# Kernel tuning notes

Hardware: AMD Instinct MI355X
Metric: run time of the kernel (lower is better)

The kernel has to match this reference:

```python
import jax, jax.numpy as jnp
import numpy as np

N_INP = 256
N_OUT = 16
H = 1024
UH = 32  # uni_hidden_unit
BATCH = 16384


def setup_inputs() -> dict:
    key = jax.random.key(0)
    ks = jax.random.split(key, 16)
    s = 0.02
    return {
        "x": jax.random.normal(ks[0], (BATCH, N_INP), dtype=jnp.float32),
        # main MLP: n_inp -> 1024 -> 1024 -> n_out
        "W0": jax.random.normal(ks[1], (N_INP, H), dtype=jnp.float32) * s,
        "b0": jnp.zeros((H,), jnp.float32),
        "W1": jax.random.normal(ks[2], (H, H), dtype=jnp.float32) * s,
        "b1": jnp.zeros((H,), jnp.float32),
        "W2": jax.random.normal(ks[3], (H, N_OUT), dtype=jnp.float32) * s,
        "b2": jnp.zeros((N_OUT,), jnp.float32),
        # stacked per-feature uni MLPs: 1 -> UH -> UH -> n_out, one per feature
        "uw1": jax.random.normal(ks[4], (N_INP, UH), dtype=jnp.float32) * s,
        "ub1": jnp.zeros((N_INP, UH), jnp.float32),
        "uw2": jax.random.normal(ks[5], (N_INP, UH, UH), dtype=jnp.float32) * s,
        "ub2": jnp.zeros((N_INP, UH), jnp.float32),
        "uw3": jax.random.normal(ks[6], (N_INP, UH, N_OUT), dtype=jnp.float32) * s,
        "ub3": jnp.zeros((N_INP, N_OUT), jnp.float32),
    }


def reference(x, W0, b0, W1, b1, W2, b2, uw1, ub1, uw2, ub2, uw3, ub3):
    # main MLP: Linear+ReLU, Linear+ReLU, Linear
    y = jax.nn.relu(x @ W0 + b0)
    y = jax.nn.relu(y @ W1 + b1)
    y = y @ W2 + b2  # [B, n_out]

    # per-feature univariate MLPs, vectorized over the feature axis i
    # input to uni MLP i is x[:, i:i+1]  -> first Linear(1, UH)
    h = jax.nn.relu(x[:, :, None] * uw1[None] + ub1[None])       # [B, I, UH]
    h = jax.nn.relu(jnp.einsum('bif,ifo->bio', h, uw2) + ub2[None])  # [B, I, UH]
    u = jnp.einsum('bif,ifo->bio', h, uw3) + ub3[None]           # [B, I, n_out]
    return y + u.sum(axis=1)
```

## Files before the change

kernel.cpp:

```cpp
#include <hip/hip_runtime.h>

typedef unsigned short u16;
typedef __attribute__((ext_vector_type(4))) float f32x4;
typedef __attribute__((ext_vector_type(4))) int i32x4;
typedef __attribute__((ext_vector_type(8))) __bf16 bf16x8;
typedef __attribute__((ext_vector_type(4))) unsigned short u16x4;

#define BATCH 16384
#define NINP 256
#define HID 1024
#define NOUT 16

__device__ __forceinline__ u16 f2bf(float f) {
  unsigned u = __builtin_bit_cast(unsigned, f);
  u += 0x7FFFu + ((u >> 16) & 1u);
  return (u16)(u >> 16);
}
__device__ __forceinline__ f32x4 mfma_bb(bf16x8 a, bf16x8 b, f32x4 c) {
  return __builtin_amdgcn_mfma_f32_16x16x32_bf16(a, b, c, 0, 0, 0);
}
__device__ __forceinline__ void gload_lds16(const void* g, void* l) {
  __builtin_amdgcn_global_load_lds(
      (const __attribute__((address_space(1))) void*)g,
      (__attribute__((address_space(3))) void*)l, 16, 0, 0);
}

static const size_t OFF_H0    = 0;
static const size_t OFF_PARTU = 0;
static const size_t OFF_XB    = 33554432;
static const size_t OFF_PARTF = 33554432;
static const size_t OFF_W0T   = 67108864;
static const size_t OFF_W1T   = 67633152;
static const size_t OFF_W2T   = 69730304;
static const size_t OFF_UWP   = 69763072;
static const size_t OFF_CB    = 70811648;

__global__ __launch_bounds__(256) void k_prep(
    const float* __restrict__ x,
    const float* __restrict__ W0, const float* __restrict__ W1,
    const float* __restrict__ W2,
    const float* __restrict__ uw1, const float* __restrict__ ub1,
    const float* __restrict__ uw2, const float* __restrict__ ub2,
    const float* __restrict__ uw3, const float* __restrict__ b2,
    const float* __restrict__ ub3,
    u16* __restrict__ xb,
    u16* __restrict__ W0T, u16* __restrict__ W1T, u16* __restrict__ W2T,
    char* __restrict__ uwp, float* __restrict__ cb)
{
  __shared__ float tile[32][33];
  const int bid = blockIdx.x;
  const int tid = threadIdx.x;

  if (bid < 1312) {
    const float* src; u16* dst; int K, N, kb, ob;
    if (bid < 256)       { src = W0; dst = W0T; K = 256;  N = 1024; int t = bid;        kb = (t & 7) * 32;  ob = (t >> 3) * 32; }
    else if (bid < 1280) { src = W1; dst = W1T; K = 1024; N = 1024; int t = bid - 256;  kb = (t & 31) * 32; ob = (t >> 5) * 32; }
    else                 { src = W2; dst = W2T; K = 1024; N = 16;   int t = bid - 1280; kb = t * 32;        ob = 0; }
    const int tx = tid & 31, ty = tid >> 5;
    for (int r = ty; r < 32; r += 8)
      if (ob + tx < N) tile[r][tx] = src[(size_t)(kb + r) * N + ob + tx];
    __syncthreads();
    for (int r = ty; r < 32; r += 8)
      if (ob + r < N) dst[(size_t)(ob + r) * K + kb + tx] = f2bf(tile[tx][r]);
  } else if (bid < 5408) {
    const int idx = ((bid - 1312) * 256 + tid) * 4;
    const float4 v = *(const float4*)&x[idx];
    u16x4 o4 = { f2bf(v.x), f2bf(v.y), f2bf(v.z), f2bf(v.w) };
    *(u16x4*)&xb[idx] = o4;
  } else if (bid < 5664) {
    const int e = ((bid - 5408) * 256 + tid) * 4;
    const float4 v = *(const float4*)&uw2[e];
    const int i = e >> 10, f = (e >> 5) & 31, o = e & 31;
    const float vv[4] = { v.x, v.y, v.z, v.w };
    u16* blob16 = (u16*)(uwp + (size_t)i * 4096);
#pragma unroll
    for (int d = 0; d < 4; ++d) {
      const int oo = o + d;
      const int lane = ((f >> 3) << 4) | (oo & 15);
      blob16[256 + (oo >> 4) * 512 + lane * 8 + (f & 7)] = f2bf(vv[d]);
    }
  } else if (bid < 5792) {
    const int e = ((bid - 5664) * 256 + tid) * 4;
    const float4 v = *(const float4*)&uw3[e];
    const int i = e >> 9, f = (e >> 4) & 31, o2 = e & 15;
    const int s = (f < 16) ? (((f >> 2) << 3) + (f & 3))
                           : ((((f - 16) >> 2) << 3) + 4 + (f & 3));
    const float vv[4] = { v.x, v.y, v.z, v.w };
    u16* blob16 = (u16*)(uwp + (size_t)i * 4096);
#pragma unroll
    for (int d = 0; d < 4; ++d)
      blob16[1280 + ((s >> 3) * 16 + o2 + d) * 8 + (s & 7)] = f2bf(vv[d]);
  } else if (bid < 5816) {
    const int e4 = (bid - 5792) * 256 + tid;
    const int i = e4 / 24, r4 = e4 % 24;
    const float* src = (r4 < 8)  ? &uw1[i * 32 + r4 * 4]
                     : (r4 < 16) ? &ub1[i * 32 + (r4 - 8) * 4]
                                 : &ub2[i * 32 + (r4 - 16) * 4];
    *(float4*)(uwp + (size_t)i * 4096 + r4 * 16) = *(const float4*)src;
  } else {
    __shared__ float red[16][16];
    const int ig = tid >> 4, o = tid & 15;
    float s = 0.f;
#pragma unroll
    for (int k = 0; k < 16; ++k) s += ub3[(ig * 16 + k) * 16 + o];
    red[ig][o] = s;
    __syncthreads();
    if (tid < 16) {
      float t = b2[tid];
#pragma unroll
      for (int k = 0; k < 16; ++k) t += red[k][tid];
      cb[tid] = t;
    }
  }
}

template<int KT, bool FOLD>
__device__ __forceinline__ void gemm_body(
    const u16* __restrict__ A, const u16* __restrict__ BT,
    const float* __restrict__ bias, u16* __restrict__ C,
    const u16* __restrict__ W2Tp, float* __restrict__ pfold, int N)
{
  extern __shared__ __align__(16) char lds[];
  const int tid = threadIdx.x;
  const int lane = tid & 63, wid = tid >> 6;
  const int l15 = lane & 15, g = lane >> 4;
  const int wA = wid >> 1;
  const int wB = wid & 1;
  const int nbn = N >> 8;
  int logical = blockIdx.x;
  { const int nwg = gridDim.x;
    if ((nwg & 7) == 0) { const int q = nwg >> 3; logical = (logical & 7) * q + (logical >> 3); } }
  const int bm = logical / nbn, bn = logical - bm * nbn;
  const size_t rb = (size_t)bm * 256, cb = (size_t)bn * 256;

  const int q7 = l15 & 7;
  const int arow0 = wA * 128 + l15;
  const int brow0 = wB * 128 + l15;

  char* const ldsA = lds;
  char* const ldsB = lds + 65536;

  const u16* Ag = A + rb * KT;
  const u16* Bg = BT + cb * KT;

  bf16x8 w2f[8];
  if constexpr (FOLD) {
#pragma unroll
    for (int c = 0; c < 8; ++c)
      w2f[c] = __builtin_bit_cast(bf16x8,
          *(const i32x4*)&W2Tp[l15 * HID + (int)cb + c * 32 + g * 8]);
  }
  float bvs[8];
#pragma unroll
  for (int n = 0; n < 8; ++n) bvs[n] = bias[cb + wB * 128 + n * 16 + l15];

  f32x4 acc[8][8] = {};
  const int NT = KT >> 6;

#define STAGE(arr, src, ktE, s) do { \
    const int G_ = (s) * 256 + tid; \
    const int row_ = G_ >> 3; \
    const int c8_ = (G_ & 7) ^ (row_ & 7); \
    gload_lds16(&(src)[(size_t)row_ * KT + (ktE) + c8_ * 8], (arr) + G_ * 16); \
  } while (0)

#define ARD(bp, m, kk) (*(const bf16x8*)((bp) + (((arow0 + (m) * 16) * 8 + (((kk) * 4 + g) ^ q7)) << 4)))
#define BRD(bp, n, kk) (*(const bf16x8*)((bp) + (((brow0 + (n) * 16) * 8 + (((kk) * 4 + g) ^ q7)) << 4)))

#define KTILE(Ab, Bb, An, Bn, kt1, LASTT) do {                                 \
    if (!(LASTT)) {                                                            \
      _Pragma("unroll")                                                        \
      for (int s = 0; s < 8; ++s) STAGE(An, Ag, kt1, s);                       \
      _Pragma("unroll")                                                        \
      for (int s = 0; s < 8; ++s) STAGE(Bn, Bg, kt1, s);                       \
    }                                                                          \
    bf16x8 a0[8], b0[8], a1[8], b1[8];                                         \
    _Pragma("unroll")                                                          \
    for (int m = 0; m < 8; ++m) a0[m] = ARD(Ab, m, 0);                         \
    _Pragma("unroll")                                                          \
    for (int n = 0; n < 8; ++n) b0[n] = BRD(Bb, n, 0);                         \
    _Pragma("unroll")                                                          \
    for (int m = 0; m < 8; ++m) a1[m] = ARD(Ab, m, 1);                         \
    _Pragma("unroll")                                                          \
    for (int n = 0; n < 8; ++n) b1[n] = BRD(Bb, n, 1);                         \
    __builtin_amdgcn_s_setprio(1);                                             \
    _Pragma("unroll")                                                          \
    for (int m = 0; m < 8; ++m)                                                \
      _Pragma("unroll")                                                        \
      for (int n = 0; n < 8; ++n)                                              \
        acc[m][n] = mfma_bb(a0[m], b0[n], acc[m][n]);                          \
    _Pragma("unroll")                                                          \
    for (int m = 0; m < 8; ++m)                                                \
      _Pragma("unroll")                                                        \
      for (int n = 0; n < 8; ++n)                                              \
        acc[m][n] = mfma_bb(a1[m], b1[n], acc[m][n]);                          \
    __builtin_amdgcn_s_setprio(0);                                             \
    asm volatile("s_waitcnt vmcnt(0)" ::: "memory");                           \
    asm volatile("s_barrier" ::: "memory");                                    \
  } while (0)

#pragma unroll
  for (int s = 0; s < 8; ++s) STAGE(ldsA, Ag, 0, s);
#pragma unroll
  for (int s = 0; s < 8; ++s) STAGE(ldsB, Bg, 0, s);
  asm volatile("s_waitcnt vmcnt(0)" ::: "memory");
  asm volatile("s_barrier" ::: "memory");

  for (int t = 0; t < NT - 1; ++t) {
    const int b = t & 1;
    KTILE(ldsA + b * 32768, ldsB + b * 32768,
          ldsA + (b ^ 1) * 32768, ldsB + (b ^ 1) * 32768,
          (t + 1) << 6, false);
  }
  {
    const int b = (NT - 1) & 1;
    KTILE(ldsA + b * 32768, ldsB + b * 32768,
          ldsA + (b ^ 1) * 32768, ldsB + (b ^ 1) * 32768, 0, true);
  }
#undef KTILE
#undef STAGE
#undef ARD
#undef BRD

  {
    char* const ep = lds;
#pragma unroll
    for (int h = 0; h < 2; ++h) {
      __syncthreads();
#pragma unroll
      for (int mloc = 0; mloc < 4; ++mloc)
#pragma unroll
        for (int n = 0; n < 8; ++n) {
          const int col = wB * 128 + n * 16 + l15;
#pragma unroll
          for (int r = 0; r < 4; ++r) {
            const int lrow = wA * 64 + mloc * 16 + g * 4 + r;
            *(u16*)(ep + lrow * 512 + ((col * 2) ^ ((lrow & 7) << 4))) =
                f2bf(fmaxf(acc[h * 4 + mloc][n][r] + bvs[n], 0.f));
          }
        }
      __syncthreads();
      if constexpr (!FOLD) {
#pragma unroll
        for (int p = 0; p < 16; ++p) {
          const int ci = p * 256 + tid;
          const int lrow = ci >> 5, c16 = ci & 31;
          const i32x4 v = *(const i32x4*)(ep + lrow * 512 + ((c16 * 16) ^ ((lrow & 7) << 4)));
          const int grow = (int)rb + (lrow >> 6) * 128 + h * 64 + (lrow & 63);
          *(i32x4*)&C[(size_t)grow * N + cb + c16 * 8] = v;
        }
      } else {
#pragma unroll
        for (int s = 0; s < 2; ++s) {
          const int lrow = wid * 32 + s * 16 + l15;
          f32x4 accf = {0.f, 0.f, 0.f, 0.f};
#pragma unroll
          for (int c = 0; c < 8; ++c) {
            const bf16x8 afr = *(const bf16x8*)(
                ep + lrow * 512 + ((c * 64 + g * 16) ^ ((lrow & 7) << 4)));
            accf = mfma_bb(afr, w2f[c], accf);
          }
          const int rowb2 = (int)rb + (wid >> 1) * 128 + h * 64 +
                            (wid & 1) * 32 + s * 16;
          float* pf = pfold + ((size_t)bn * BATCH + rowb2) * NOUT;
#pragma unroll
          for (int r = 0; r < 4; ++r)
            pf[(g * 4 + r) * NOUT + l15] = accf[r];
        }
      }
    }
  }
}

__global__ __launch_bounds__(256, 1) void k_g1(
    const u16* __restrict__ A, const u16* __restrict__ BT,
    const float* __restrict__ bias, u16* __restrict__ C, int N)
{
  gemm_body<256, false>(A, BT, bias, C, nullptr, nullptr, N);
}
__global__ __launch_bounds__(256, 1) void k_g2(
    const u16* __restrict__ A, const u16* __restrict__ BT,
    const float* __restrict__ bias, const u16* __restrict__ W2Tp,
    float* __restrict__ pfold, int N)
{
  gemm_body<1024, true>(A, BT, bias, nullptr, W2Tp, pfold, N);
}

__global__ __launch_bounds__(256, 4) void k_uni(
    const float* __restrict__ x,
    const char* __restrict__ uwp,
    float* __restrict__ part)
{
  const int tid = threadIdx.x, lane = tid & 63, wid = tid >> 6;
  const int l15 = lane & 15, g = lane >> 4;
  const int chunk = blockIdx.x & 7, rowblk = blockIdx.x >> 3;
  const int rb_blk = rowblk * 128;
  const int rb = rb_blk + wid * 32;
  const int i0 = chunk * 32;

  __shared__ __align__(16) float xt[128][33];
  __shared__ __align__(16) char wbuf[3][4096];

  {
    const int r0 = tid >> 3, c4 = (tid & 7) << 2;
#pragma unroll
    for (int rr = 0; rr < 128; rr += 32)
      *(float4*)&xt[rr + r0][c4] =
          *(const float4*)&x[(size_t)(rb_blk + rr + r0) * NINP + i0 + c4];
  }
  gload_lds16(uwp + (size_t)i0 * 4096 + tid * 16, &wbuf[0][tid * 16]);
  gload_lds16(uwp + (size_t)(i0 + 1) * 4096 + tid * 16, &wbuf[1][tid * 16]);
  __syncthreads();

  const f32x4 zero4 = {0.f, 0.f, 0.f, 0.f};
  f32x4 acc0 = zero4, acc1 = zero4;
  const float* xr0 = &xt[wid * 32 + l15][0];
  const float* xr1 = &xt[wid * 32 + 16 + l15][0];

#pragma unroll 2
  for (int ii = 0; ii < 32; ++ii) {
    const int nf = i0 + ((ii + 2) & 31);
    gload_lds16(uwp + (size_t)nf * 4096 + tid * 16,
                &wbuf[(ii + 2) % 3][tid * 16]);

    const char* bp = &wbuf[ii % 3][0];
    const f32x4 w1lo = *(const f32x4*)(bp + g * 32);
    const f32x4 w1hi = *(const f32x4*)(bp + g * 32 + 16);
    const f32x4 b1lo = *(const f32x4*)(bp + 128 + g * 32);
    const f32x4 b1hi = *(const f32x4*)(bp + 128 + g * 32 + 16);
    const f32x4 bb0  = *(const f32x4*)(bp + 256 + g * 16);
    const f32x4 bb1  = *(const f32x4*)(bp + 320 + g * 16);
    const bf16x8 bv0 = *(const bf16x8*)(bp + 512 + lane * 16);
    const bf16x8 bv1 = *(const bf16x8*)(bp + 1536 + lane * 16);
    const bf16x8 b3  = *(const bf16x8*)(bp + 2560 + lane * 16);
    const float xv0 = xr0[ii], xv1 = xr1[ii];

    bf16x8 af0, af1;
#pragma unroll
    for (int j = 0; j < 4; ++j) {
      af0[j]     = (__bf16)fmaxf(fmaf(xv0, w1lo[j], b1lo[j]), 0.f);
      af0[4 + j] = (__bf16)fmaxf(fmaf(xv0, w1hi[j], b1hi[j]), 0.f);
      af1[j]     = (__bf16)fmaxf(fmaf(xv1, w1lo[j], b1lo[j]), 0.f);
      af1[4 + j] = (__bf16)fmaxf(fmaf(xv1, w1hi[j], b1hi[j]), 0.f);
    }

    const f32x4 d00 = mfma_bb(bv0, af0, bb0);
    const f32x4 d10 = mfma_bb(bv1, af0, bb1);
    const f32x4 d01 = mfma_bb(bv0, af1, bb0);
    const f32x4 d11 = mfma_bb(bv1, af1, bb1);

    bf16x8 h20, h21;
#pragma unroll
    for (int j = 0; j < 4; ++j) {
      h20[j]     = (__bf16)fmaxf(d00[j], 0.f);
      h20[4 + j] = (__bf16)fmaxf(d10[j], 0.f);
      h21[j]     = (__bf16)fmaxf(d01[j], 0.f);
      h21[4 + j] = (__bf16)fmaxf(d11[j], 0.f);
    }

    acc0 = mfma_bb(b3, h20, acc0);
    acc1 = mfma_bb(b3, h21, acc1);

    asm volatile("s_waitcnt vmcnt(1)" ::: "memory");
    __builtin_amdgcn_s_barrier();
  }

  float* p = part + ((size_t)chunk * BATCH + rb) * NOUT;
  *(f32x4*)&p[l15 * 16 + g * 4] = acc0;
  *(f32x4*)&p[(16 + l15) * 16 + g * 4] = acc1;
}

__global__ __launch_bounds__(256) void k_reduce(
    const float* __restrict__ pu, const float* __restrict__ pf,
    const float* __restrict__ cb, float* __restrict__ out)
{
  const int j4 = blockIdx.x * 256 + threadIdx.x;
  const float4 c = ((const float4*)cb)[j4 & 3];
  const float4* a4 = (const float4*)pu;
  const float4* b4 = (const float4*)pf;
  float rx = c.x, ry = c.y, rz = c.z, rw = c.w;
#pragma unroll
  for (int cc = 0; cc < 8; ++cc) {
    const float4 a = a4[cc * 65536 + j4];
    rx += a.x; ry += a.y; rz += a.z; rw += a.w;
  }
#pragma unroll
  for (int cc = 0; cc < 4; ++cc) {
    const float4 a = b4[cc * 65536 + j4];
    rx += a.x; ry += a.y; rz += a.z; rw += a.w;
  }
  float4 r; r.x = rx; r.y = ry; r.z = rz; r.w = rw;
  ((float4*)out)[j4] = r;
}

extern "C" void kernel_launch(void* const* d_in, const int* in_sizes, int n_in,
                              void* d_out, int out_size, void* d_ws, size_t ws_size,
                              hipStream_t stream) {
  (void)in_sizes; (void)n_in; (void)out_size; (void)ws_size;
  const float* x   = (const float*)d_in[0];
  const float* W0  = (const float*)d_in[1];
  const float* b0  = (const float*)d_in[2];
  const float* W1  = (const float*)d_in[3];
  const float* b1  = (const float*)d_in[4];
  const float* W2  = (const float*)d_in[5];
  const float* b2  = (const float*)d_in[6];
  const float* uw1 = (const float*)d_in[7];
  const float* ub1 = (const float*)d_in[8];
  const float* uw2 = (const float*)d_in[9];
  const float* ub2 = (const float*)d_in[10];
  const float* uw3 = (const float*)d_in[11];
  const float* ub3 = (const float*)d_in[12];
  float* out = (float*)d_out;

  char* ws = (char*)d_ws;
  u16*   H0    = (u16*)(ws + OFF_H0);
  u16*   xb    = (u16*)(ws + OFF_XB);
  u16*   W0T   = (u16*)(ws + OFF_W0T);
  u16*   W1T   = (u16*)(ws + OFF_W1T);
  u16*   W2T   = (u16*)(ws + OFF_W2T);
  char*  uwp   = (char*)(ws + OFF_UWP);
  float* cb    = (float*)(ws + OFF_CB);
  float* partu = (float*)(ws + OFF_PARTU);
  float* partf = (float*)(ws + OFF_PARTF);

  hipFuncSetAttribute((const void*)k_g1,
                      hipFuncAttributeMaxDynamicSharedMemorySize, 131072);
  hipFuncSetAttribute((const void*)k_g2,
                      hipFuncAttributeMaxDynamicSharedMemorySize, 131072);

  k_prep<<<5817, 256, 0, stream>>>(x, W0, W1, W2, uw1, ub1, uw2, ub2, uw3,
                                   b2, ub3, xb, W0T, W1T, W2T, uwp, cb);
  k_g1<<<256, 256, 131072, stream>>>(xb, W0T, b0, H0, HID);
  k_g2<<<256, 256, 131072, stream>>>(H0, W1T, b1, W2T, partf, HID);
  k_uni<<<1024, 256, 0, stream>>>(x, uwp, partu);
  k_reduce<<<256, 256, 0, stream>>>(partu, partf, cb, out);
}
```

Measured before the change: 100.9 us.

## Shrink GEMM tiles to 128x128 single-buffered with higher occupancy

The two MLP GEMM kernels move from 256x256 tiles with double-buffered 128KB dynamic LDS and BK=64 to 128x128 tiles with a 32KB static LDS buffer, BK=32, and a simple sync-load-compute loop. Launch bounds allow 3 blocks per CU and the grid grows to 1024 blocks. The folded W2 epilogue now writes 8 column-block partials, so the reduce loop is widened to match. The aim is more occupancy and parallelism to hide latency, at the cost of less data reuse per tile, no explicit load/compute overlap, and more partial-sum traffic.

```diff
diff --git a/kernel.cpp b/kernel.cpp
--- a/kernel.cpp
+++ b/kernel.cpp
@@ -120,165 +120,118 @@
     const float* __restrict__ bias, u16* __restrict__ C,
     const u16* __restrict__ W2Tp, float* __restrict__ pfold, int N)
 {
-  extern __shared__ __align__(16) char lds[];
+  __shared__ __align__(16) char smem[32768];
+  char* const As = smem;
+  char* const Bs = smem + 8192;
+
   const int tid = threadIdx.x;
   const int lane = tid & 63, wid = tid >> 6;
   const int l15 = lane & 15, g = lane >> 4;
-  const int wA = wid >> 1;
-  const int wB = wid & 1;
-  const int nbn = N >> 8;
+  const int wr = (wid >> 1) * 64, wc = (wid & 1) * 64;
+  const int nbn = N >> 7;
   int logical = blockIdx.x;
   { const int nwg = gridDim.x;
     if ((nwg & 7) == 0) { const int q = nwg >> 3; logical = (logical & 7) * q + (logical >> 3); } }
   const int bm = logical / nbn, bn = logical - bm * nbn;
-  const size_t rb = (size_t)bm * 256, cb = (size_t)bn * 256;
-
-  const int q7 = l15 & 7;
-  const int arow0 = wA * 128 + l15;
-  const int brow0 = wB * 128 + l15;
-
-  char* const ldsA = lds;
-  char* const ldsB = lds + 65536;
+  const size_t rb = (size_t)bm * 128, cb = (size_t)bn * 128;
 
   const u16* Ag = A + rb * KT;
   const u16* Bg = BT + cb * KT;
 
-  bf16x8 w2f[8];
+  bf16x8 w2f[4];
   if constexpr (FOLD) {
 #pragma unroll
-    for (int c = 0; c < 8; ++c)
+    for (int c = 0; c < 4; ++c)
       w2f[c] = __builtin_bit_cast(bf16x8,
           *(const i32x4*)&W2Tp[l15 * HID + (int)cb + c * 32 + g * 8]);
   }
-  float bvs[8];
-#pragma unroll
-  for (int n = 0; n < 8; ++n) bvs[n] = bias[cb + wB * 128 + n * 16 + l15];
-
-  f32x4 acc[8][8] = {};
-  const int NT = KT >> 6;
-
-#define STAGE(arr, src, ktE, s) do { \
+  float bv[4];
+#pragma unroll
+  for (int n = 0; n < 4; ++n) bv[n] = bias[cb + wc + n * 16 + l15];
+
+  f32x4 acc[4][4] = {};
+
+#define STAGE(arr, src, kt, s) do { \
     const int G_ = (s) * 256 + tid; \
-    const int row_ = G_ >> 3; \
-    const int c8_ = (G_ & 7) ^ (row_ & 7); \
-    gload_lds16(&(src)[(size_t)row_ * KT + (ktE) + c8_ * 8], (arr) + G_ * 16); \
+    const int row_ = G_ >> 2; \
+    const int srcg_ = (G_ & 3) ^ ((row_ >> 1) & 3); \
+    gload_lds16(&(src)[(size_t)row_ * KT + (kt) + srcg_ * 8], (arr) + G_ * 16); \
   } while (0)
 
-#define ARD(bp, m, kk) (*(const bf16x8*)((bp) + (((arow0 + (m) * 16) * 8 + (((kk) * 4 + g) ^ q7)) << 4)))
-#define BRD(bp, n, kk) (*(const bf16x8*)((bp) + (((brow0 + (n) * 16) * 8 + (((kk) * 4 + g) ^ q7)) << 4)))
-
-#define KTILE(Ab, Bb, An, Bn, kt1, LASTT) do {                                 \
-    if (!(LASTT)) {                                                            \
-      _Pragma("unroll")                                                        \
-      for (int s = 0; s < 8; ++s) STAGE(An, Ag, kt1, s);                       \
-      _Pragma("unroll")                                                        \
-      for (int s = 0; s < 8; ++s) STAGE(Bn, Bg, kt1, s);                       \
-    }                                                                          \
-    bf16x8 a0[8], b0[8], a1[8], b1[8];                                         \
-    _Pragma("unroll")                                                          \
-    for (int m = 0; m < 8; ++m) a0[m] = ARD(Ab, m, 0);                         \
-    _Pragma("unroll")                                                          \
-    for (int n = 0; n < 8; ++n) b0[n] = BRD(Bb, n, 0);                         \
-    _Pragma("unroll")                                                          \
-    for (int m = 0; m < 8; ++m) a1[m] = ARD(Ab, m, 1);                         \
-    _Pragma("unroll")                                                          \
-    for (int n = 0; n < 8; ++n) b1[n] = BRD(Bb, n, 1);                         \
-    __builtin_amdgcn_s_setprio(1);                                             \
-    _Pragma("unroll")                                                          \
-    for (int m = 0; m < 8; ++m)                                                \
-      _Pragma("unroll")                                                        \
-      for (int n = 0; n < 8; ++n)                                              \
-        acc[m][n] = mfma_bb(a0[m], b0[n], acc[m][n]);                          \
-    _Pragma("unroll")                                                          \
-    for (int m = 0; m < 8; ++m)                                                \
-      _Pragma("unroll")                                                        \
-      for (int n = 0; n < 8; ++n)                                              \
-        acc[m][n] = mfma_bb(a1[m], b1[n], acc[m][n]);                          \
-    __builtin_amdgcn_s_setprio(0);                                             \
-    asm volatile("s_waitcnt vmcnt(0)" ::: "memory");                           \
-    asm volatile("s_barrier" ::: "memory");                                    \
-  } while (0)
-
-#pragma unroll
-  for (int s = 0; s < 8; ++s) STAGE(ldsA, Ag, 0, s);
-#pragma unroll
-  for (int s = 0; s < 8; ++s) STAGE(ldsB, Bg, 0, s);
-  asm volatile("s_waitcnt vmcnt(0)" ::: "memory");
-  asm volatile("s_barrier" ::: "memory");
-
-  for (int t = 0; t < NT - 1; ++t) {
-    const int b = t & 1;
-    KTILE(ldsA + b * 32768, ldsB + b * 32768,
-          ldsA + (b ^ 1) * 32768, ldsB + (b ^ 1) * 32768,
-          (t + 1) << 6, false);
-  }
+#define FRD(bp, r0) (*(const bf16x8*)((bp) + ((r0) << 6) + ((g ^ (((r0) >> 1) & 3)) << 4)))
+
+  for (int kt = 0; kt < KT; kt += 32) {
+    STAGE(As, Ag, kt, 0); STAGE(As, Ag, kt, 1);
+    STAGE(Bs, Bg, kt, 0); STAGE(Bs, Bg, kt, 1);
+    __syncthreads();
+    bf16x8 a[4], b[4];
+#pragma unroll
+    for (int m = 0; m < 4; ++m) a[m] = FRD(As, wr + m * 16 + l15);
+#pragma unroll
+    for (int n = 0; n < 4; ++n) b[n] = FRD(Bs, wc + n * 16 + l15);
+    __builtin_amdgcn_s_setprio(1);
+#pragma unroll
+    for (int m = 0; m < 4; ++m)
+#pragma unroll
+      for (int n = 0; n < 4; ++n)
+        acc[m][n] = mfma_bb(a[m], b[n], acc[m][n]);
+    __builtin_amdgcn_s_setprio(0);
+    __syncthreads();
+  }
+#undef STAGE
+#undef FRD
+
   {
-    const int b = (NT - 1) & 1;
-    KTILE(ldsA + b * 32768, ldsB + b * 32768,
-          ldsA + (b ^ 1) * 32768, ldsB + (b ^ 1) * 32768, 0, true);
-  }
-#undef KTILE
-#undef STAGE
-#undef ARD
-#undef BRD
-
-  {
-    char* const ep = lds;
-#pragma unroll
-    for (int h = 0; h < 2; ++h) {
-      __syncthreads();
-#pragma unroll
-      for (int mloc = 0; mloc < 4; ++mloc)
-#pragma unroll
-        for (int n = 0; n < 8; ++n) {
-          const int col = wB * 128 + n * 16 + l15;
-#pragma unroll
-          for (int r = 0; r < 4; ++r) {
-            const int lrow = wA * 64 + mloc * 16 + g * 4 + r;
-            *(u16*)(ep + lrow * 512 + ((col * 2) ^ ((lrow & 7) << 4))) =
-                f2bf(fmaxf(acc[h * 4 + mloc][n][r] + bvs[n], 0.f));
-          }
-        }
-      __syncthreads();
-      if constexpr (!FOLD) {
-#pragma unroll
-        for (int p = 0; p < 16; ++p) {
-          const int ci = p * 256 + tid;
-          const int lrow = ci >> 5, c16 = ci & 31;
-          const i32x4 v = *(const i32x4*)(ep + lrow * 512 + ((c16 * 16) ^ ((lrow & 7) << 4)));
-          const int grow = (int)rb + (lrow >> 6) * 128 + h * 64 + (lrow & 63);
-          *(i32x4*)&C[(size_t)grow * N + cb + c16 * 8] = v;
-        }
-      } else {
-#pragma unroll
-        for (int s = 0; s < 2; ++s) {
-          const int lrow = wid * 32 + s * 16 + l15;
-          f32x4 accf = {0.f, 0.f, 0.f, 0.f};
-#pragma unroll
-          for (int c = 0; c < 8; ++c) {
-            const bf16x8 afr = *(const bf16x8*)(
-                ep + lrow * 512 + ((c * 64 + g * 16) ^ ((lrow & 7) << 4)));
-            accf = mfma_bb(afr, w2f[c], accf);
-          }
-          const int rowb2 = (int)rb + (wid >> 1) * 128 + h * 64 +
-                            (wid & 1) * 32 + s * 16;
-          float* pf = pfold + ((size_t)bn * BATCH + rowb2) * NOUT;
-#pragma unroll
-          for (int r = 0; r < 4; ++r)
-            pf[(g * 4 + r) * NOUT + l15] = accf[r];
+    char* const ep = smem;
+    __syncthreads();
+#pragma unroll
+    for (int m = 0; m < 4; ++m)
+#pragma unroll
+      for (int n = 0; n < 4; ++n) {
+        const int col = wc + n * 16 + l15;
+#pragma unroll
+        for (int r = 0; r < 4; ++r) {
+          const int lrow = wr + m * 16 + g * 4 + r;
+          *(u16*)(ep + lrow * 256 + ((col * 2) ^ ((lrow & 7) << 4))) =
+              f2bf(fmaxf(acc[m][n][r] + bv[n], 0.f));
         }
       }
-    }
-  }
-}
-
-__global__ __launch_bounds__(256, 1) void k_g1(
+    __syncthreads();
+    if constexpr (!FOLD) {
+#pragma unroll
+      for (int p = 0; p < 8; ++p) {
+        const int ci = p * 256 + tid;
+        const int lrow = ci >> 4, c16 = ci & 15;
+        const i32x4 v = *(const i32x4*)(ep + lrow * 256 + ((c16 * 16) ^ ((lrow & 7) << 4)));
+        *(i32x4*)&C[(size_t)((int)rb + lrow) * N + cb + c16 * 8] = v;
+      }
+    } else {
+#pragma unroll
+      for (int s = 0; s < 2; ++s) {
+        const int lrow = wid * 32 + s * 16 + l15;
+        f32x4 accf = {0.f, 0.f, 0.f, 0.f};
+#pragma unroll
+        for (int c = 0; c < 4; ++c) {
+          const bf16x8 afr = *(const bf16x8*)(
+              ep + lrow * 256 + ((c * 64 + g * 16) ^ ((lrow & 7) << 4)));
+          accf = mfma_bb(afr, w2f[c], accf);
+        }
+        float* pf = pfold + ((size_t)bn * BATCH + rb + wid * 32 + s * 16) * NOUT;
+#pragma unroll
+        for (int r = 0; r < 4; ++r)
+          pf[(g * 4 + r) * NOUT + l15] = accf[r];
+      }
+    }
+  }
+}
+
+__global__ __launch_bounds__(256, 3) void k_g1(
     const u16* __restrict__ A, const u16* __restrict__ BT,
     const float* __restrict__ bias, u16* __restrict__ C, int N)
 {
   gemm_body<256, false>(A, BT, bias, C, nullptr, nullptr, N);
 }
-__global__ __launch_bounds__(256, 1) void k_g2(
+__global__ __launch_bounds__(256, 3) void k_g2(
     const u16* __restrict__ A, const u16* __restrict__ BT,
     const float* __restrict__ bias, const u16* __restrict__ W2Tp,
     float* __restrict__ pfold, int N)
@@ -385,7 +338,7 @@
     rx += a.x; ry += a.y; rz += a.z; rw += a.w;
   }
 #pragma unroll
-  for (int cc = 0; cc < 4; ++cc) {
+  for (int cc = 0; cc < 8; ++cc) {
     const float4 a = b4[cc * 65536 + j4];
     rx += a.x; ry += a.y; rz += a.z; rw += a.w;
   }
@@ -423,15 +376,10 @@
   float* partu = (float*)(ws + OFF_PARTU);
   float* partf = (float*)(ws + OFF_PARTF);
 
-  hipFuncSetAttribute((const void*)k_g1,
-                      hipFuncAttributeMaxDynamicSharedMemorySize, 131072);
-  hipFuncSetAttribute((const void*)k_g2,
-                      hipFuncAttributeMaxDynamicSharedMemorySize, 131072);
-
   k_prep<<<5817, 256, 0, stream>>>(x, W0, W1, W2, uw1, ub1, uw2, ub2, uw3,
                                    b2, ub3, xb, W0T, W1T, W2T, uwp, cb);
-  k_g1<<<256, 256, 131072, stream>>>(xb, W0T, b0, H0, HID);
-  k_g2<<<256, 256, 131072, stream>>>(H0, W1T, b1, W2T, partf, HID);
+  k_g1<<<1024, 256, 0, stream>>>(xb, W0T, b0, H0, HID);
+  k_g2<<<1024, 256, 0, stream>>>(H0, W1T, b1, W2T, partf, HID);
   k_uni<<<1024, 256, 0, stream>>>(x, uwp, partu);
   k_reduce<<<256, 256, 0, stream>>>(partu, partf, cb, out);
 }
```

New measurement: 111.0 us (median of 2 runs). 9.9% more time.
